# Performance work log

Hardware: AMD Instinct MI355X
Metric: run time of the kernel (lower is better)

The kernel has to match this reference:

```python
import jax, jax.numpy as jnp
import numpy as np

K = 3        # kernel_size
STRIDE = 1
PAD = 1
BASIS = 8    # act_fun.get_size()


def cheb_basis(x):
    """Chebyshev polynomial basis T_0..T_{BASIS-1} of tanh(x); appends basis axis."""
    t = jnp.tanh(x)
    polys = [jnp.ones_like(t), t]
    for _ in range(BASIS - 2):
        polys.append(2.0 * t * polys[-1] - polys[-2])
    return jnp.stack(polys, axis=-1)  # (..., BASIS)


def silu(x):
    return x * jax.nn.sigmoid(x)


def unfold(x):
    """torch F.unfold equivalent: (b,c,h,w) -> (b, c, K*K, L), L = ho*wo."""
    b, c, h, w = x.shape
    ho = (h - K + 2 * PAD) // STRIDE + 1
    wo = (w - K + 2 * PAD) // STRIDE + 1
    xp = jnp.pad(x, ((0, 0), (0, 0), (PAD, PAD), (PAD, PAD)))
    pats = [xp[:, :, i:i + STRIDE * ho:STRIDE, j:j + STRIDE * wo:STRIDE]
            for i in range(K) for j in range(K)]
    pats = jnp.stack(pats, axis=2)  # (b, c, K*K, ho, wo)
    return pats.reshape(b, c, K * K, ho * wo), ho, wo


def setup_inputs() -> dict:
    key = jax.random.key(0)
    k1, k2, k3 = jax.random.split(key, 3)
    cin, cout = 64, 64
    x = jax.random.normal(k1, (16, cin, 32, 32), dtype=jnp.float32)
    # xavier_normal_ on (in,out,k^2,1): std = sqrt(2/(fan_in+fan_out)) approx
    w = jax.random.normal(k2, (cin, cout, K * K), dtype=jnp.float32) * jnp.sqrt(2.0 / (cin + cout))
    # normal_(c, 0, 0.1) on (in,out,k^2,1,basis) -> squeeze the broadcast dim
    c = jax.random.normal(k3, (cin, cout, K * K, BASIS), dtype=jnp.float32) * 0.1
    return {"x": x, "w": w, "c": c}


def reference(x, w, c):
    b = x.shape[0]
    pats, ho, wo = unfold(x)          # (b, i, k, l)
    res = silu(pats)                  # residual activation path
    act = cheb_basis(pats)            # (b, i, k, l, s) spline basis
    # sum_i sum_k w[i,o,k] * res[b,i,k,l]
    term1 = jnp.einsum('iok,bikl->bol', w, res)
    # sum_i sum_k sum_s w[i,o,k]*c[i,o,k,s]*act[b,i,k,l,s] (fused, avoids (b,i,o,k,l,s))
    cw = c * w[..., None]             # (i, o, k, s)
    term2 = jnp.einsum('ioks,bikls->bol', cw, act)
    return (term1 + term2).reshape(b, -1, ho, wo)
```

## Files before the change

### kernel.cpp

```cpp
#include <hip/hip_runtime.h>
#include <hip/hip_bf16.h>


#define CIN   64
#define COUT  64
#define HW    32
#define LL    1024
#define NS    8

typedef __attribute__((ext_vector_type(8))) short short8;
typedef __attribute__((ext_vector_type(4))) float f32x4;


__global__ void prep_kernel(const float* __restrict__ w,
                            const float* __restrict__ c,
                            __hip_bfloat16* __restrict__ Wt,
                            float* __restrict__ bias,
                            const float* __restrict__ x,
                            float* __restrict__ dummy) {
    const int bx = blockIdx.x;
    if (bx < 144) {
        const int tid = bx * 256 + threadIdx.x;
        const int i = tid / (9 * COUT);
        const int r = tid - i * 9 * COUT;
        const int k = r / COUT;
        const int o = r - k * COUT;
        const int widx = (i * COUT + o) * 9 + k;
        const float wv = w[widx];
        __hip_bfloat16* dst = Wt + (size_t)tid * NS;
        dst[0] = __float2bfloat16(wv);
#pragma unroll
        for (int s = 1; s < 8; ++s) dst[s] = __float2bfloat16(wv * c[widx * 8 + s]);
        return;
    }
    if (bx < 208) {
        const int o = bx - 144;
        const int i = threadIdx.x;
        if (i >= 64) return;
        float v = 0.f;
#pragma unroll
        for (int k = 0; k < 9; ++k) {
            const int idx = (i * COUT + o) * 9 + k;
            v += w[idx] * c[idx * 8];
        }
#pragma unroll
        for (int off = 32; off > 0; off >>= 1) v += __shfl_down(v, off);
        if (i == 0) bias[o] = v;
        return;
    }
    const int idx = bx - 208;
    const int r  = idx & 7;
    const int m  = idx >> 3;
    const int b  = r + 8 * (m & 1);
    const int ch = m >> 1;
    const float4 v = ((const float4*)(x + (size_t)(b * CIN + ch) * LL))[threadIdx.x];
    const float acc = v.x + v.y + v.z + v.w;
    if (acc == 1.0e-37f) dummy[threadIdx.x] = acc;
}

__global__ __launch_bounds__(512, 2) void kan_fused_kernel(
        const float* __restrict__ x,
        const __hip_bfloat16* __restrict__ Wt,
        const float* __restrict__ bias,
        float* __restrict__ out) {
    __shared__ __align__(16) unsigned short Wlds[52224];

    const int tid   = threadIdx.x;
    const int wv    = tid >> 6;
    const int lane  = tid & 63;
    const int quad  = lane >> 4;
    const int l16   = lane & 15;
    const int kq    = wv >> 1;
    const int oh    = wv & 1;

    const int b    = blockIdx.x;
    const int row0 = blockIdx.y << 1;

    const unsigned short* WtU = (const unsigned short*)Wt;
    float* xf = (float*)Wlds;

#pragma unroll
    for (int p = 0; p < 17; ++p) {
        const int cell = p * 512 + tid;
        const int ch  = cell / 136;
        const int pos = cell - ch * 136;
        const int r4  = pos / 34;
        const int col = pos - r4 * 34;
        const int gy  = row0 - 1 + r4;
        const int gx  = col - 1;
        float v = 0.f;
        if ((unsigned)gy < 32u && (unsigned)gx < 32u)
            v = x[((size_t)(b * CIN + ch) * HW + gy) * HW + gx];
        xf[cell] = v;
    }
    __syncthreads();

    f32x4 acc[4][2];
#pragma unroll
    for (int h = 0; h < 4; ++h)
#pragma unroll
        for (int nt = 0; nt < 2; ++nt) acc[h][nt] = (f32x4){0.f, 0.f, 0.f, 0.f};

    for (int chunk = 0; chunk < 4; ++chunk) {
        const int chbase = kq * 16 + chunk * 4;
        unsigned short* usd = Wlds + 17408 + (chunk & 1) * 17408 + kq * 4352;

#pragma unroll
        for (int p = 0; p < 5; ++p) {
            const int cell = (p * 2 + oh) * 64 + lane;
            if (cell < 544) {
                const int ch  = cell & 3;
                const int pos = cell >> 2;
                const float xv = xf[(chbase + ch) * 136 + pos];
                const float e   = __expf(xv);
                const float sig = e * __builtin_amdgcn_rcpf(1.f + e);
                const float res = xv * sig;
                const float t   = 1.f - 2.f * __builtin_amdgcn_rcpf(__builtin_fmaf(e, e, 1.f));
                const float t2  = t + t;
                const float T2 = __builtin_fmaf(t2, t,  -1.f);
                const float T3 = __builtin_fmaf(t2, T2, -t);
                const float T4 = __builtin_fmaf(t2, T3, -T2);
                const float T5 = __builtin_fmaf(t2, T4, -T3);
                const float T6 = __builtin_fmaf(t2, T5, -T4);
                const float T7 = __builtin_fmaf(t2, T6, -T5);
                union { __hip_bfloat162 h2[4]; float4 f4; } U;
                U.h2[0] = __float22bfloat162_rn(make_float2(res, t));
                U.h2[1] = __float22bfloat162_rn(make_float2(T2, T3));
                U.h2[2] = __float22bfloat162_rn(make_float2(T4, T5));
                U.h2[3] = __float22bfloat162_rn(make_float2(T6, T7));
                *(float4*)(usd + cell * 8) = U.f4;
            }
        }
        __syncthreads();

        const unsigned short* wchunk = WtU +
            ((size_t)(chbase + quad) * 9 * COUT + (oh << 5) + l16) * NS;
#pragma unroll
        for (int kpos = 0; kpos < 9; ++kpos) {
            const int dy = kpos / 3 - 1, dx = kpos % 3 - 1;
            const int posb = (dy + 1) * 34 + (dx + 1);
            short8 af0 = *(const short8*)(usd + (((posb      + l16) * 4 + quad)) * 8);
            short8 af1 = *(const short8*)(usd + (((posb + 16 + l16) * 4 + quad)) * 8);
            short8 af2 = *(const short8*)(usd + (((posb + 34 + l16) * 4 + quad)) * 8);
            short8 af3 = *(const short8*)(usd + (((posb + 50 + l16) * 4 + quad)) * 8);
#pragma unroll
            for (int nt = 0; nt < 2; ++nt) {
                short8 wf = *(const short8*)(wchunk + (kpos * COUT + nt * 16) * NS);
                acc[0][nt] = __builtin_amdgcn_mfma_f32_16x16x32_bf16(wf, af0, acc[0][nt], 0, 0, 0);
                acc[1][nt] = __builtin_amdgcn_mfma_f32_16x16x32_bf16(wf, af1, acc[1][nt], 0, 0, 0);
                acc[2][nt] = __builtin_amdgcn_mfma_f32_16x16x32_bf16(wf, af2, acc[2][nt], 0, 0, 0);
                acc[3][nt] = __builtin_amdgcn_mfma_f32_16x16x32_bf16(wf, af3, acc[3][nt], 0, 0, 0);
            }
        }
    }

    float* red = (float*)Wlds;
#pragma unroll
    for (int h = 0; h < 4; ++h)
#pragma unroll
        for (int nt = 0; nt < 2; ++nt)
#pragma unroll
            for (int r = 0; r < 4; ++r) {
                const int p = h * 16 + l16;
                const int o = (oh << 5) + nt * 16 + quad * 4 + r;
                red[(kq * 64 + p) * 65 + o] = acc[h][nt][r];
            }
    __syncthreads();

#pragma unroll
    for (int rep = 0; rep < 8; ++rep) {
        const int v = rep * 512 + tid;
        const int p = v & 63;
        const int o = v >> 6;
        const float s = red[p * 65 + o] + red[(64 + p) * 65 + o]
                      + red[(128 + p) * 65 + o] + red[(192 + p) * 65 + o] + bias[o];
        out[(size_t)(b * COUT + o) * LL + (row0 + (p >> 5)) * HW + (p & 31)] = s;
    }
}

extern "C" void kernel_launch(void* const* d_in, const int* in_sizes, int n_in,
                              void* d_out, int out_size, void* d_ws, size_t ws_size,
                              hipStream_t stream) {
    const float* x = (const float*)d_in[0];
    const float* w = (const float*)d_in[1];
    const float* c = (const float*)d_in[2];
    float* out = (float*)d_out;

    char* ws = (char*)d_ws;
    __hip_bfloat16* Wt    = (__hip_bfloat16*)(ws);
    float*          bias  = (float*)(ws + 589824);
    float*          dummy = (float*)(ws + 590080);

    prep_kernel<<<1232, 256, 0, stream>>>(w, c, Wt, bias, x, dummy);
    kan_fused_kernel<<<dim3(16, 16), 512, 0, stream>>>(x, Wt, bias, out);
}
```

Measured before the change: 79.66 us.

## Double block to 1024 threads, splitting output channels across four waves

The fused KAN kernel now runs 16 waves per block instead of 8. Each wave covers 16 output channels rather than 32, so it keeps one accumulator tile set and issues half as many MFMAs. The aim is more waves in flight to hide LDS and global latency, with the basis-expansion and staging work spread across more threads. In exchange, each A-fragment LDS read feeds fewer MFMAs, so more LDS traffic is spent per useful MFMA. The larger block also loads the register budget through the new launch bound.

Result: faster. 74.10 us (-7.0%).

```diff
diff --git a/kernel.cpp b/kernel.cpp
--- a/kernel.cpp
+++ b/kernel.cpp
@@ -58,7 +58,7 @@
     if (acc == 1.0e-37f) dummy[threadIdx.x] = acc;
 }
 
-__global__ __launch_bounds__(512, 2) void kan_fused_kernel(
+__global__ __launch_bounds__(1024, 4) void kan_fused_kernel(
         const float* __restrict__ x,
         const __hip_bfloat16* __restrict__ Wt,
         const float* __restrict__ bias,
@@ -70,8 +70,8 @@
     const int lane  = tid & 63;
     const int quad  = lane >> 4;
     const int l16   = lane & 15;
-    const int kq    = wv >> 1;
-    const int oh    = wv & 1;
+    const int kq    = wv >> 2;
+    const int oq    = wv & 3;
 
     const int b    = blockIdx.x;
     const int row0 = blockIdx.y << 1;
@@ -80,34 +80,34 @@
     float* xf = (float*)Wlds;
 
 #pragma unroll
-    for (int p = 0; p < 17; ++p) {
-        const int cell = p * 512 + tid;
-        const int ch  = cell / 136;
-        const int pos = cell - ch * 136;
-        const int r4  = pos / 34;
-        const int col = pos - r4 * 34;
-        const int gy  = row0 - 1 + r4;
-        const int gx  = col - 1;
-        float v = 0.f;
-        if ((unsigned)gy < 32u && (unsigned)gx < 32u)
-            v = x[((size_t)(b * CIN + ch) * HW + gy) * HW + gx];
-        xf[cell] = v;
+    for (int p = 0; p < 9; ++p) {
+        const int cell = p * 1024 + tid;
+        if (cell < 8704) {
+            const int ch  = cell / 136;
+            const int pos = cell - ch * 136;
+            const int r4  = pos / 34;
+            const int col = pos - r4 * 34;
+            const int gy  = row0 - 1 + r4;
+            const int gx  = col - 1;
+            float v = 0.f;
+            if ((unsigned)gy < 32u && (unsigned)gx < 32u)
+                v = x[((size_t)(b * CIN + ch) * HW + gy) * HW + gx];
+            xf[cell] = v;
+        }
     }
     __syncthreads();
 
-    f32x4 acc[4][2];
+    f32x4 acc[4];
 #pragma unroll
-    for (int h = 0; h < 4; ++h)
-#pragma unroll
-        for (int nt = 0; nt < 2; ++nt) acc[h][nt] = (f32x4){0.f, 0.f, 0.f, 0.f};
+    for (int h = 0; h < 4; ++h) acc[h] = (f32x4){0.f, 0.f, 0.f, 0.f};
 
     for (int chunk = 0; chunk < 4; ++chunk) {
         const int chbase = kq * 16 + chunk * 4;
         unsigned short* usd = Wlds + 17408 + (chunk & 1) * 17408 + kq * 4352;
 
 #pragma unroll
-        for (int p = 0; p < 5; ++p) {
-            const int cell = (p * 2 + oh) * 64 + lane;
+        for (int p = 0; p < 3; ++p) {
+            const int cell = (p * 4 + oq) * 64 + lane;
             if (cell < 544) {
                 const int ch  = cell & 3;
                 const int pos = cell >> 2;
@@ -134,7 +134,7 @@
         __syncthreads();
 
         const unsigned short* wchunk = WtU +
-            ((size_t)(chbase + quad) * 9 * COUT + (oh << 5) + l16) * NS;
+            ((size_t)(chbase + quad) * 9 * COUT + (oq << 4) + l16) * NS;
 #pragma unroll
         for (int kpos = 0; kpos < 9; ++kpos) {
             const int dy = kpos / 3 - 1, dx = kpos % 3 - 1;
@@ -143,14 +143,11 @@
             short8 af1 = *(const short8*)(usd + (((posb + 16 + l16) * 4 + quad)) * 8);
             short8 af2 = *(const short8*)(usd + (((posb + 34 + l16) * 4 + quad)) * 8);
             short8 af3 = *(const short8*)(usd + (((posb + 50 + l16) * 4 + quad)) * 8);
-#pragma unroll
-            for (int nt = 0; nt < 2; ++nt) {
-                short8 wf = *(const short8*)(wchunk + (kpos * COUT + nt * 16) * NS);
-                acc[0][nt] = __builtin_amdgcn_mfma_f32_16x16x32_bf16(wf, af0, acc[0][nt], 0, 0, 0);
-                acc[1][nt] = __builtin_amdgcn_mfma_f32_16x16x32_bf16(wf, af1, acc[1][nt], 0, 0, 0);
-                acc[2][nt] = __builtin_amdgcn_mfma_f32_16x16x32_bf16(wf, af2, acc[2][nt], 0, 0, 0);
-                acc[3][nt] = __builtin_amdgcn_mfma_f32_16x16x32_bf16(wf, af3, acc[3][nt], 0, 0, 0);
-            }
+            short8 wf = *(const short8*)(wchunk + kpos * COUT * NS);
+            acc[0] = __builtin_amdgcn_mfma_f32_16x16x32_bf16(wf, af0, acc[0], 0, 0, 0);
+            acc[1] = __builtin_amdgcn_mfma_f32_16x16x32_bf16(wf, af1, acc[1], 0, 0, 0);
+            acc[2] = __builtin_amdgcn_mfma_f32_16x16x32_bf16(wf, af2, acc[2], 0, 0, 0);
+            acc[3] = __builtin_amdgcn_mfma_f32_16x16x32_bf16(wf, af3, acc[3], 0, 0, 0);
         }
     }
 
@@ -158,18 +155,16 @@
 #pragma unroll
     for (int h = 0; h < 4; ++h)
 #pragma unroll
-        for (int nt = 0; nt < 2; ++nt)
-#pragma unroll
-            for (int r = 0; r < 4; ++r) {
-                const int p = h * 16 + l16;
-                const int o = (oh << 5) + nt * 16 + quad * 4 + r;
-                red[(kq * 64 + p) * 65 + o] = acc[h][nt][r];
-            }
+        for (int r = 0; r < 4; ++r) {
+            const int p = h * 16 + l16;
+            const int o = (oq << 4) + quad * 4 + r;
+            red[(kq * 64 + p) * 65 + o] = acc[h][r];
+        }
     __syncthreads();
 
 #pragma unroll
-    for (int rep = 0; rep < 8; ++rep) {
-        const int v = rep * 512 + tid;
+    for (int rep = 0; rep < 4; ++rep) {
+        const int v = rep * 1024 + tid;
         const int p = v & 63;
         const int o = v >> 6;
         const float s = red[p * 65 + o] + red[(64 + p) * 65 + o]
@@ -192,5 +187,5 @@
     float*          dummy = (float*)(ws + 590080);
 
     prep_kernel<<<1232, 256, 0, stream>>>(w, c, Wt, bias, x, dummy);
-    kan_fused_kernel<<<dim3(16, 16), 512, 0, stream>>>(x, Wt, bias, out);
+    kan_fused_kernel<<<dim3(16, 16), 1024, 0, stream>>>(x, Wt, bias, out);
 }
```
